# Optimization experiments

Hardware: AMD Instinct MI355X
Metric: run time of the kernel (lower is better)

Reference implementation:

```python
import jax, jax.numpy as jnp
import numpy as np

K_SIZE = 5


def _extract_patches(x, k):
    """x: [n, b, h, w, c] -> [n, b, h, w, k*k, c] with zero SAME padding.

    Matches tf.image.extract_patches row-major patch ordering with channels
    fastest, as consumed by the Reshape((H, W, k*k, Ci)) in the original.
    """
    p = k // 2
    n, b, h, w, c = x.shape
    xp = jnp.pad(x, ((0, 0), (0, 0), (p, p), (p, p), (0, 0)))
    shifts = [xp[:, :, i:i + h, j:j + w, :] for i in range(k) for j in range(k)]
    return jnp.stack(shifts, axis=4)


def setup_inputs() -> dict:
    key = jax.random.key(0)
    k1, k2, k3, k4 = jax.random.split(key, 4)
    B, H, W, C = 4, 128, 128, 64
    heads, Ci = 4, 16  # intermediate_dim=64, head_num=4
    main = jax.random.normal(k1, (B, H, W, C), jnp.float32)
    ref = jax.random.normal(k2, (B, H, W, C), jnp.float32)
    he_std = np.sqrt(2.0 / C).astype(np.float32)  # he_normal, fan_in=C (1x1 conv)
    w_main = jax.random.normal(k3, (heads, C, Ci), jnp.float32) * he_std
    w_ref = jax.random.normal(k4, (heads, C, Ci), jnp.float32) * he_std
    return {"main": main, "ref": ref, "w_main": w_main, "w_ref": w_ref}


def reference(main, ref, w_main, w_ref):
    # per-head 1x1 convs (no bias): [n,b,h,w,d]
    q = jnp.einsum('bhwc,ncd->nbhwd', main, w_main)
    r = jnp.einsum('bhwc,ncd->nbhwd', ref, w_ref)
    patches = _extract_patches(r, K_SIZE)          # [n,b,h,w,k*k,d]
    attn = jnp.einsum('nbhwd,nbhwkd->nbhwk', q, patches)
    attn = jax.nn.softmax(attn, axis=-1)           # softmax over k*k neighbors
    return jnp.mean(attn, axis=0)                  # average over heads -> [b,h,w,k*k]
```

## Files before the change

kernel.cpp:

```cpp
#include <hip/hip_runtime.h>
#include <hip/hip_bf16.h>

typedef _Float16 f16;
typedef f16 f16x2 __attribute__((ext_vector_type(2)));
typedef f16 f16x4 __attribute__((ext_vector_type(4)));
typedef f16 f16x8 __attribute__((ext_vector_type(8)));
typedef float f32x4 __attribute__((ext_vector_type(4)));

constexpr int B_  = 4;
constexpr int H_  = 128;
constexpr int W_  = 128;
constexpr int C_  = 64;
constexpr int NH_ = 4;
constexpr int D_  = 16;
constexpr int KK_ = 25;

constexpr int TW_  = 8, TH_ = 8;
constexpr int HWID = 12, HHEI = 12;
constexpr int NPX  = HHEI * HWID;
constexpr int MOFF  = NPX * 64 * 2;
constexpr int MXOFF = 27648;
constexpr int SMOFF = 29696;
constexpr int SMEM  = 31744;
constexpr int PSTRIDE = KK_ + 2;
constexpr int PSLAB   = 64 * PSTRIDE;

#if __has_builtin(__builtin_amdgcn_fdot2)
#define FDOT2(a, b, c) __builtin_amdgcn_fdot2((a), (b), (c), false)
#else
#define FDOT2(a, b, c) fmaf((float)(a)[1], (float)(b)[1], fmaf((float)(a)[0], (float)(b)[0], (c)))
#endif

__device__ __forceinline__ int div12(int x) { return (x * 171) >> 11; }

__global__ __launch_bounds__(512, 8) void rl8mh7(
    const float* __restrict__ mainp, const float* __restrict__ refp,
    const float* __restrict__ wmain, const float* __restrict__ wref,
    float* __restrict__ out)
{
    __shared__ __align__(16) unsigned char smraw[SMEM];
    f16*   abuf  = (f16*)smraw;
    f16*   mabuf = (f16*)(smraw + MOFF);
    float* xbuf  = (float*)smraw;
    float* mxbuf = (float*)(smraw + MXOFF);
    float* smbuf = (float*)(smraw + SMOFF);

    const int tid = threadIdx.x;
    const int l   = tid & 63;
    const int wid = __builtin_amdgcn_readfirstlane(tid >> 6);
    const int n   = wid & 3;
    const int h   = wid >> 2;
    const int row = l & 15;
    const int kg  = l >> 4;

    const int x0 = blockIdx.x * TW_;
    const int y0 = blockIdx.y * TH_;
    const int b  = blockIdx.z;
    const float* mainb = mainp + ((size_t)b * H_) * W_ * C_;
    const float* refb  = refp  + ((size_t)b * H_) * W_ * C_;

    f16x8 am[2], ar[2];
    {
        const float* wm = wmain + n * C_ * D_;
        const float* wr = wref  + n * C_ * D_;
        #pragma unroll
        for (int s = 0; s < 2; ++s) {
            union { f16x8 v; f16 e[8]; } um, ur;
            #pragma unroll
            for (int i = 0; i < 8; ++i) {
                int k = s * 32 + kg * 8 + i;
                um.e[i] = (f16)wm[k * D_ + row];
                ur.e[i] = (f16)wr[k * D_ + row];
            }
            am[s] = um.v; ar[s] = ur.v;
        }
    }

    for (int j = tid; j < NPX * 16; j += 512) {
        int hp = j >> 4, c4 = j & 15;
        int hy = div12(hp), hx = hp - hy * HWID;
        int gy = y0 + hy - 2, gx = x0 + hx - 2;
        float4 v = make_float4(0.f, 0.f, 0.f, 0.f);
        if ((unsigned)gy < (unsigned)H_ && (unsigned)gx < (unsigned)W_)
            v = *(const float4*)(refb + ((size_t)gy * W_ + gx) * C_ + c4 * 4);
        f16x4 h4 = {(f16)v.x, (f16)v.y, (f16)v.z, (f16)v.w};
        int off = hp * 64 + ((((c4 >> 1) ^ (hp & 7)) << 3) | ((c4 & 1) << 2));
        *(f16x4*)(abuf + off) = h4;
    }
    for (int j = tid; j < 64 * 16; j += 512) {
        int px = j >> 4, c4 = j & 15;
        int gy = y0 + (px >> 3), gx = x0 + (px & 7);
        float4 v = *(const float4*)(mainb + ((size_t)gy * W_ + gx) * C_ + c4 * 4);
        f16x4 h4 = {(f16)v.x, (f16)v.y, (f16)v.z, (f16)v.w};
        int off = px * 64 + ((((c4 >> 1) ^ (px & 7)) << 3) | ((c4 & 1) << 2));
        *(f16x4*)(mabuf + off) = h4;
    }
    __syncthreads();

    auto proj = [&](const f16* src, int t, const f16x8* A) -> f16x4 {
        int px = t * 16 + row;
        const f16* rp = src + px * 64;
        f16x8 B0 = *(const f16x8*)(rp + (((kg     ^ (px & 7)) << 3)));
        f16x8 B1 = *(const f16x8*)(rp + ((((kg+4) ^ (px & 7)) << 3)));
        f32x4 acc = {0.f, 0.f, 0.f, 0.f};
        acc = __builtin_amdgcn_mfma_f32_16x16x32_f16(A[0], B0, acc, 0, 0, 0);
        acc = __builtin_amdgcn_mfma_f32_16x16x32_f16(A[1], B1, acc, 0, 0, 0);
        return f16x4{(f16)acc[0], (f16)acc[1], (f16)acc[2], (f16)acc[3]};
    };
    f16x4 racc0, racc1, racc2, racc3, racc4, qacc0, qacc1;
    if (h == 0) {
        racc0 = proj(abuf, 0, ar); racc1 = proj(abuf, 2, ar);
        racc2 = proj(abuf, 4, ar); racc3 = proj(abuf, 6, ar);
        racc4 = proj(abuf, 8, ar);
        qacc0 = proj(mabuf, 0, am); qacc1 = proj(mabuf, 2, am);
    } else {
        racc0 = proj(abuf, 1, ar); racc1 = proj(abuf, 3, ar);
        racc2 = proj(abuf, 5, ar); racc3 = proj(abuf, 7, ar);
        qacc0 = proj(mabuf, 1, am); qacc1 = proj(mabuf, 3, am);
    }
    __syncthreads();

    auto wrout = [&](f16* dst, int t, f16x4 v) {
        int px = t * 16 + row;
        int c16 = (n << 1) | (kg >> 1);
        int off = px * 64 + (((c16 ^ (px & 7)) << 3) | ((kg & 1) << 2));
        *(f16x4*)(dst + off) = v;
    };
    if (h == 0) {
        wrout(abuf, 0, racc0); wrout(abuf, 2, racc1); wrout(abuf, 4, racc2);
        wrout(abuf, 6, racc3); wrout(abuf, 8, racc4);
        wrout(mabuf, 0, qacc0); wrout(mabuf, 2, qacc1);
    } else {
        wrout(abuf, 1, racc0); wrout(abuf, 3, racc1); wrout(abuf, 5, racc2);
        wrout(abuf, 7, racc3);
        wrout(mabuf, 1, qacc0); wrout(mabuf, 3, qacc1);
    }
    __syncthreads();

    const int py  = l >> 3;
    const int pxx = l & 7;
    f16x8 q0 = *(const f16x8*)(mabuf + l * 64 + ((((n << 1) | 0) ^ (l & 7)) << 3));
    f16x8 q1 = *(const f16x8*)(mabuf + l * 64 + ((((n << 1) | 1) ^ (l & 7)) << 3));
    const f16x2* q2a = (const f16x2*)&q0;
    const f16x2* q2b = (const f16x2*)&q1;

    float lg[13];
    auto do_lg = [&](int idx, int k) {
        int ky = k / 5, kx = k % 5;
        int np = (py + ky) * 12 + pxx + kx;
        const f16* rp = abuf + np * 64;
        f16x8 r0 = *(const f16x8*)(rp + ((((n << 1) | 0) ^ (np & 7)) << 3));
        f16x8 r1 = *(const f16x8*)(rp + ((((n << 1) | 1) ^ (np & 7)) << 3));
        const f16x2* r2a = (const f16x2*)&r0;
        const f16x2* r2b = (const f16x2*)&r1;
        float a = 0.f;
        #pragma unroll
        for (int j = 0; j < 4; ++j) a = FDOT2(q2a[j], r2a[j], a);
        #pragma unroll
        for (int j = 0; j < 4; ++j) a = FDOT2(q2b[j], r2b[j], a);
        lg[idx] = a;
    };
    if (h == 0) {
        do_lg(0,0);  do_lg(1,1);  do_lg(2,2);  do_lg(3,3);  do_lg(4,4);
        do_lg(5,5);  do_lg(6,6);  do_lg(7,7);  do_lg(8,8);  do_lg(9,9);
        do_lg(10,10); do_lg(11,11); do_lg(12,12);
    } else {
        do_lg(0,13); do_lg(1,14); do_lg(2,15); do_lg(3,16); do_lg(4,17);
        do_lg(5,18); do_lg(6,19); do_lg(7,20); do_lg(8,21); do_lg(9,22);
        do_lg(10,23); do_lg(11,24);
        lg[12] = -1e30f;
    }

    float mloc = lg[0];
    #pragma unroll
    for (int k = 1; k < 13; ++k) mloc = fmaxf(mloc, lg[k]);
    mxbuf[(h * 4 + n) * 64 + l] = mloc;
    __syncthreads();
    float mo = mxbuf[((1 - h) * 4 + n) * 64 + l];
    float m  = fmaxf(mloc, mo);

    float s = 0.f;
    #pragma unroll
    for (int k = 0; k < 13; ++k) { lg[k] = __expf(lg[k] - m); s += lg[k]; }
    smbuf[(h * 4 + n) * 64 + l] = s;
    __syncthreads();
    float so  = smbuf[((1 - h) * 4 + n) * 64 + l];
    float inv = 1.0f / (s + so);

    const int k0 = h * 13;
    #pragma unroll
    for (int k = 0; k < 13; ++k) {
        if (k0 + k < KK_)
            xbuf[n * PSLAB + l * PSTRIDE + (k0 + k)] = lg[k] * inv;
    }
    __syncthreads();

    for (int i = tid; i < TW_ * TH_ * KK_; i += 512) {
        int p2 = i / KK_;
        int k  = i - p2 * KK_;
        int off = p2 * PSTRIDE + k;
        float v = 0.25f * (xbuf[off] + xbuf[PSLAB + off] + xbuf[2 * PSLAB + off] + xbuf[3 * PSLAB + off]);
        out[(((size_t)b * H_ + (y0 + (p2 >> 3))) * W_ + (x0 + (p2 & 7))) * KK_ + k] = v;
    }
}

extern "C" void kernel_launch(void* const* d_in, const int* in_sizes, int n_in,
                              void* d_out, int out_size, void* d_ws, size_t ws_size,
                              hipStream_t stream) {
    const float* mainp = (const float*)d_in[0];
    const float* refp  = (const float*)d_in[1];
    const float* wmain = (const float*)d_in[2];
    const float* wref  = (const float*)d_in[3];
    float* outp = (float*)d_out;

    dim3 grid(W_ / TW_, H_ / TH_, B_);
    rl8mh7<<<grid, dim3(512), 0, stream>>>(mainp, refp, wmain, wref, outp);
}
```

Measured before the change: 19.78 us.

## Merge softmax max/sum exchange into one barrier, swizzle tiles, defer weight loads

The two-wave softmax now exchanges a local max and an unnormalized sum together in one packed float2 and rescales online. This removes one block-wide barrier and one shared-memory round trip. The block index is swizzled so neighbouring workgroups cover different tile rows, the weight fragments are loaded after the input staging to lower register pressure, and the exponentials are held in half precision. Storing exponentials as f16 adds rounding error to the output probabilities.

```diff
diff --git a/kernel.cpp b/kernel.cpp
--- a/kernel.cpp
+++ b/kernel.cpp
@@ -19,8 +19,7 @@
 constexpr int HWID = 12, HHEI = 12;
 constexpr int NPX  = HHEI * HWID;
 constexpr int MOFF  = NPX * 64 * 2;
-constexpr int MXOFF = 27648;
-constexpr int SMOFF = 29696;
+constexpr int MSOFF = 27648;
 constexpr int SMEM  = 31744;
 constexpr int PSTRIDE = KK_ + 2;
 constexpr int PSLAB   = 64 * PSTRIDE;
@@ -33,17 +32,16 @@
 
 __device__ __forceinline__ int div12(int x) { return (x * 171) >> 11; }
 
-__global__ __launch_bounds__(512, 8) void rl8mh7(
+__global__ __launch_bounds__(512, 8) void rl8mh8(
     const float* __restrict__ mainp, const float* __restrict__ refp,
     const float* __restrict__ wmain, const float* __restrict__ wref,
     float* __restrict__ out)
 {
     __shared__ __align__(16) unsigned char smraw[SMEM];
-    f16*   abuf  = (f16*)smraw;
-    f16*   mabuf = (f16*)(smraw + MOFF);
-    float* xbuf  = (float*)smraw;
-    float* mxbuf = (float*)(smraw + MXOFF);
-    float* smbuf = (float*)(smraw + SMOFF);
+    f16*    abuf  = (f16*)smraw;
+    f16*    mabuf = (f16*)(smraw + MOFF);
+    float*  xbuf  = (float*)smraw;
+    float2* msbuf = (float2*)(smraw + MSOFF);
 
     const int tid = threadIdx.x;
     const int l   = tid & 63;
@@ -53,28 +51,13 @@
     const int row = l & 15;
     const int kg  = l >> 4;
 
-    const int x0 = blockIdx.x * TW_;
-    const int y0 = blockIdx.y * TH_;
+    const int bid = blockIdx.y * 16 + blockIdx.x;
+    const int swz = (bid & 7) * 32 + (bid >> 3);
+    const int x0 = (swz & 15) * TW_;
+    const int y0 = (swz >> 4) * TH_;
     const int b  = blockIdx.z;
     const float* mainb = mainp + ((size_t)b * H_) * W_ * C_;
     const float* refb  = refp  + ((size_t)b * H_) * W_ * C_;
-
-    f16x8 am[2], ar[2];
-    {
-        const float* wm = wmain + n * C_ * D_;
-        const float* wr = wref  + n * C_ * D_;
-        #pragma unroll
-        for (int s = 0; s < 2; ++s) {
-            union { f16x8 v; f16 e[8]; } um, ur;
-            #pragma unroll
-            for (int i = 0; i < 8; ++i) {
-                int k = s * 32 + kg * 8 + i;
-                um.e[i] = (f16)wm[k * D_ + row];
-                ur.e[i] = (f16)wr[k * D_ + row];
-            }
-            am[s] = um.v; ar[s] = ur.v;
-        }
-    }
 
     for (int j = tid; j < NPX * 16; j += 512) {
         int hp = j >> 4, c4 = j & 15;
@@ -97,6 +80,18 @@
     }
     __syncthreads();
 
+    auto build_w = [&](const float* wsrc, f16x8* A) {
+        const float* w = wsrc + n * C_ * D_;
+        #pragma unroll
+        for (int s = 0; s < 2; ++s) {
+            union { f16x8 v; f16 e[8]; } u;
+            #pragma unroll
+            for (int i = 0; i < 8; ++i)
+                u.e[i] = (f16)w[(s * 32 + kg * 8 + i) * D_ + row];
+            A[s] = u.v;
+        }
+    };
+
     auto proj = [&](const f16* src, int t, const f16x8* A) -> f16x4 {
         int px = t * 16 + row;
         const f16* rp = src + px * 64;
@@ -108,15 +103,23 @@
         return f16x4{(f16)acc[0], (f16)acc[1], (f16)acc[2], (f16)acc[3]};
     };
     f16x4 racc0, racc1, racc2, racc3, racc4, qacc0, qacc1;
-    if (h == 0) {
-        racc0 = proj(abuf, 0, ar); racc1 = proj(abuf, 2, ar);
-        racc2 = proj(abuf, 4, ar); racc3 = proj(abuf, 6, ar);
-        racc4 = proj(abuf, 8, ar);
-        qacc0 = proj(mabuf, 0, am); qacc1 = proj(mabuf, 2, am);
-    } else {
-        racc0 = proj(abuf, 1, ar); racc1 = proj(abuf, 3, ar);
-        racc2 = proj(abuf, 5, ar); racc3 = proj(abuf, 7, ar);
-        qacc0 = proj(mabuf, 1, am); qacc1 = proj(mabuf, 3, am);
+    {
+        f16x8 ar[2];
+        build_w(wref, ar);
+        if (h == 0) {
+            racc0 = proj(abuf, 0, ar); racc1 = proj(abuf, 2, ar);
+            racc2 = proj(abuf, 4, ar); racc3 = proj(abuf, 6, ar);
+            racc4 = proj(abuf, 8, ar);
+        } else {
+            racc0 = proj(abuf, 1, ar); racc1 = proj(abuf, 3, ar);
+            racc2 = proj(abuf, 5, ar); racc3 = proj(abuf, 7, ar);
+        }
+    }
+    {
+        f16x8 am[2];
+        build_w(wmain, am);
+        if (h == 0) { qacc0 = proj(mabuf, 0, am); qacc1 = proj(mabuf, 2, am); }
+        else        { qacc0 = proj(mabuf, 1, am); qacc1 = proj(mabuf, 3, am); }
     }
     __syncthreads();
 
@@ -174,24 +177,37 @@
     float mloc = lg[0];
     #pragma unroll
     for (int k = 1; k < 13; ++k) mloc = fmaxf(mloc, lg[k]);
-    mxbuf[(h * 4 + n) * 64 + l] = mloc;
-    __syncthreads();
-    float mo = mxbuf[((1 - h) * 4 + n) * 64 + l];
-    float m  = fmaxf(mloc, mo);
 
     float s = 0.f;
+    f16x2 pk[7];
     #pragma unroll
-    for (int k = 0; k < 13; ++k) { lg[k] = __expf(lg[k] - m); s += lg[k]; }
-    smbuf[(h * 4 + n) * 64 + l] = s;
-    __syncthreads();
-    float so  = smbuf[((1 - h) * 4 + n) * 64 + l];
-    float inv = 1.0f / (s + so);
-
-    const int k0 = h * 13;
-    #pragma unroll
-    for (int k = 0; k < 13; ++k) {
-        if (k0 + k < KK_)
-            xbuf[n * PSLAB + l * PSTRIDE + (k0 + k)] = lg[k] * inv;
+    for (int j = 0; j < 6; ++j) {
+        float e0 = __expf(lg[2*j]   - mloc);
+        float e1 = __expf(lg[2*j+1] - mloc);
+        s += e0 + e1;
+        pk[j] = f16x2{(f16)e0, (f16)e1};
+    }
+    {
+        float e12 = __expf(lg[12] - mloc);
+        s += e12;
+        pk[6] = f16x2{(f16)e12, (f16)0.f};
+    }
+    msbuf[(h * 4 + n) * 64 + l] = make_float2(mloc, s);
+    __syncthreads();
+    float2 o = msbuf[((1 - h) * 4 + n) * 64 + l];
+    float m    = fmaxf(mloc, o.x);
+    float sc   = __expf(mloc - m);
+    float osc  = __expf(o.x  - m);
+    float inv  = sc / (s * sc + o.y * osc);
+
+    {
+        float* dst = &xbuf[n * PSLAB + l * PSTRIDE + h * 13];
+        #pragma unroll
+        for (int j = 0; j < 6; ++j) {
+            dst[2*j]     = (float)pk[j][0] * inv;
+            dst[2*j + 1] = (float)pk[j][1] * inv;
+        }
+        if (h == 0) dst[12] = (float)pk[6][0] * inv;
     }
     __syncthreads();
 
@@ -214,5 +230,5 @@
     float* outp = (float*)d_out;
 
     dim3 grid(W_ / TW_, H_ / TH_, B_);
-    rl8mh7<<<grid, dim3(512), 0, stream>>>(mainp, refp, wmain, wref, outp);
+    rl8mh8<<<grid, dim3(512), 0, stream>>>(mainp, refp, wmain, wref, outp);
 }
```

Result: faster. 18.88 us (-4.6%).
